# Optimization experiments

Measured on AMD Instinct MI355X. Metric: run time of the kernel, lower is better.

The kernel has to match this reference:

```python
import jax, jax.numpy as jnp
import numpy as np
import math

FREQS = jnp.array([1., 2., 4., 8., 7., 5.], dtype=jnp.float32)  # default frequencies


def setup_inputs() -> dict:
    key = jax.random.key(0)
    k1, k2, k3 = jax.random.split(key, 3)
    B, N, H, F = 8, 4096, 256, 6
    x = jax.random.normal(k1, (B, N, H), dtype=jnp.float32)
    t = jax.random.uniform(k2, (B, 1), dtype=jnp.float32) * (2.0 * math.pi)
    oscillators = jax.random.normal(k3, (F, H, H), dtype=jnp.float32) * 0.1
    # phase_shifts[i] = i / F * pi, broadcast over hidden dim (matches torch init)
    phase_shifts = jnp.broadcast_to(
        (jnp.arange(F, dtype=jnp.float32) / F * math.pi)[:, None], (F, H)
    ).copy()
    return {"x": x, "t": t, "oscillators": oscillators, "phase_shifts": phase_shifts}


def reference(x, t, oscillators, phase_shifts):
    # resonator[b, f, h] = sin(freq_f * t[b, 0] + phase[f, h])
    res = jnp.sin(FREQS[None, :, None] * t[:, :, None] + phase_shifts[None, :, :])  # [B, F, H]
    # result[b, n, k] = sum_f (x[b, n, :] @ W_f)[k] * res[b, f, k]
    return jnp.einsum('bnh,fhk,bfk->bnk', x, oscillators, res)
```

## Files before the change

kernel.cpp:

```cpp
#include <hip/hip_runtime.h>
#include <hip/hip_bf16.h>


#define B_  8
#define N_  4096
#define H_  256

typedef __attribute__((ext_vector_type(8))) short s8v;
typedef __attribute__((ext_vector_type(4))) float f4v;

__global__ __launch_bounds__(256) void build_w(
    const float* __restrict__ osc,
    const float* __restrict__ t,
    const float* __restrict__ phase,
    __hip_bfloat16* __restrict__ Wt)
{
    const float freqs[6] = {1.f, 2.f, 4.f, 8.f, 7.f, 5.f};
    __shared__ float tr[16 * 68];

    const int b  = blockIdx.z;
    const int n0 = blockIdx.y * 64;
    const int h0 = blockIdx.x * 128;
    const int tid = threadIdx.x;

    const float tb = t[b];
    const int nr = (tid & 15) * 4;
    const int hr = tid >> 4;
    float s[6][4];
#pragma unroll
    for (int f = 0; f < 6; ++f)
#pragma unroll
        for (int j = 0; j < 4; ++j)
            s[f][j] = __sinf(freqs[f] * tb + phase[f * 256 + n0 + nr + j]);

    const int nw = tid >> 2;
    const int hw = (tid & 3) * 4;
    __hip_bfloat16* wout = Wt + (size_t)b * 65536 + (size_t)(n0 + nw) * 256 + h0;

    for (int hp = 0; hp < 8; ++hp) {
        const int h = h0 + hp * 16 + hr;
        float4 acc = make_float4(0.f, 0.f, 0.f, 0.f);
#pragma unroll
        for (int f = 0; f < 6; ++f) {
            float4 o = *(const float4*)&osc[f * 65536 + h * 256 + n0 + nr];
            acc.x += o.x * s[f][0];
            acc.y += o.y * s[f][1];
            acc.z += o.z * s[f][2];
            acc.w += o.w * s[f][3];
        }
        __syncthreads();
        *(float4*)&tr[hr * 68 + nr] = acc;
        __syncthreads();
        float v0 = tr[(hw + 0) * 68 + nw];
        float v1 = tr[(hw + 1) * 68 + nw];
        float v2 = tr[(hw + 2) * 68 + nw];
        float v3 = tr[(hw + 3) * 68 + nw];
        union { __hip_bfloat162 h2[2]; unsigned long long q; } cv;
        cv.h2[0] = __float22bfloat162_rn(make_float2(v0, v1));
        cv.h2[1] = __float22bfloat162_rn(make_float2(v2, v3));
        *(unsigned long long*)(wout + hp * 16 + hw) = cv.q;
    }
}

#define LDST 40

__global__ __launch_bounds__(512, 4) void gemm(
    const float* __restrict__ X,
    const __hip_bfloat16* __restrict__ Wt,
    float* __restrict__ out)
{
    __shared__ short As[64 * LDST];
    __shared__ short Bs[256 * LDST];

    const int b     = blockIdx.y;
    const int mTile = blockIdx.x;

    const int tid    = threadIdx.x;
    const int lane   = tid & 63;
    const int wave   = tid >> 6;
    const int lane15 = lane & 15;
    const int quad   = lane >> 4;
    const int wm     = wave >> 2;
    const int wn     = wave & 3;

    const float* Xb          = X   + (size_t)b * N_ * H_ + (size_t)mTile * 64 * H_;
    const __hip_bfloat16* Wb = Wt  + (size_t)b * H_ * H_;
    float* Ob                = out + (size_t)b * N_ * H_ + (size_t)mTile * 64 * H_;

    const int arow = tid >> 3;
    const int aseg = tid & 7;
    const float* pa = Xb + (size_t)arow * H_ + aseg * 4;

    const int brow = tid >> 1;
    const int bh   = tid & 1;
    const __hip_bfloat16* pb = Wb + (size_t)brow * H_ + bh * 16;

    f4v acc[2][4] = {};

    float4 av = *(const float4*)pa;
    uint4  bv0 = *(const uint4*)(pb);
    uint4  bv1 = *(const uint4*)(pb + 8);

    for (int it = 0; it < 8; ++it) {
        union { __hip_bfloat162 h2[2]; unsigned long long q; } cv;
        cv.h2[0] = __float22bfloat162_rn(make_float2(av.x, av.y));
        cv.h2[1] = __float22bfloat162_rn(make_float2(av.z, av.w));
        *(unsigned long long*)(&As[arow * LDST + aseg * 4]) = cv.q;
        *(uint4*)(&Bs[brow * LDST + bh * 16 + 0]) = bv0;
        *(uint4*)(&Bs[brow * LDST + bh * 16 + 8]) = bv1;
        __syncthreads();

        if (it < 7) {
            av  = *(const float4*)(pa + (it + 1) * 32);
            bv0 = *(const uint4*)(pb + (it + 1) * 32);
            bv1 = *(const uint4*)(pb + (it + 1) * 32 + 8);
        }

        s8v af[2], bf[4];
#pragma unroll
        for (int mt = 0; mt < 2; ++mt)
            af[mt] = *(const s8v*)(&As[(wm * 32 + mt * 16 + lane15) * LDST + quad * 8]);
#pragma unroll
        for (int nt = 0; nt < 4; ++nt)
            bf[nt] = *(const s8v*)(&Bs[(wn * 64 + nt * 16 + lane15) * LDST + quad * 8]);

#pragma unroll
        for (int mt = 0; mt < 2; ++mt)
#pragma unroll
            for (int nt = 0; nt < 4; ++nt)
                acc[mt][nt] = __builtin_amdgcn_mfma_f32_16x16x32_bf16(
                    af[mt], bf[nt], acc[mt][nt], 0, 0, 0);
        __syncthreads();
    }

#pragma unroll
    for (int mt = 0; mt < 2; ++mt) {
#pragma unroll
        for (int r = 0; r < 4; ++r) {
            int row = wm * 32 + mt * 16 + quad * 4 + r;
            float* po = Ob + (size_t)row * H_ + wn * 64 + lane15;
#pragma unroll
            for (int nt = 0; nt < 4; ++nt)
                po[nt * 16] = acc[mt][nt][r];
        }
    }
}

extern "C" void kernel_launch(void* const* d_in, const int* in_sizes, int n_in,
                              void* d_out, int out_size, void* d_ws, size_t ws_size,
                              hipStream_t stream) {
    const float* x     = (const float*)d_in[0];
    const float* t     = (const float*)d_in[1];
    const float* osc   = (const float*)d_in[2];
    const float* phase = (const float*)d_in[3];
    __hip_bfloat16* Wt = (__hip_bfloat16*)d_ws;
    float* out = (float*)d_out;

    dim3 gw(2, 4, 8);
    build_w<<<gw, 256, 0, stream>>>(osc, t, phase, Wt);

    dim3 gg(64, 8);
    gemm<<<gg, 512, 0, stream>>>(x, Wt, out);
}
```

Before: 101.3 us.

## Load MFMA fragments directly from global memory, bypassing LDS staging

The GEMM now has each lane load its A and B MFMA fragments straight from global memory into registers and convert A to bf16 in place. This removes the shared-memory tiles and both __syncthreads per K step. The cost is redundant global loads: each X row is read by all 4 wn waves and each W row by both wm waves, which relies on L1/L2 to absorb the duplication. Global access patterns also become 32-byte segments spread across rows, and register use grows from holding next-iteration prefetches.

```diff
diff --git a/kernel.cpp b/kernel.cpp
--- a/kernel.cpp
+++ b/kernel.cpp
@@ -62,16 +62,20 @@
     }
 }
 
-#define LDST 40
+__device__ __forceinline__ s8v cvt_frag(float4 lo, float4 hi) {
+    union { __hip_bfloat162 h2[4]; s8v v; } cv;
+    cv.h2[0] = __float22bfloat162_rn(make_float2(lo.x, lo.y));
+    cv.h2[1] = __float22bfloat162_rn(make_float2(lo.z, lo.w));
+    cv.h2[2] = __float22bfloat162_rn(make_float2(hi.x, hi.y));
+    cv.h2[3] = __float22bfloat162_rn(make_float2(hi.z, hi.w));
+    return cv.v;
+}
 
 __global__ __launch_bounds__(512, 4) void gemm(
     const float* __restrict__ X,
     const __hip_bfloat16* __restrict__ Wt,
     float* __restrict__ out)
 {
-    __shared__ short As[64 * LDST];
-    __shared__ short Bs[256 * LDST];
-
     const int b     = blockIdx.y;
     const int mTile = blockIdx.x;
 
@@ -83,54 +87,59 @@
     const int wm     = wave >> 2;
     const int wn     = wave & 3;
 
-    const float* Xb          = X   + (size_t)b * N_ * H_ + (size_t)mTile * 64 * H_;
-    const __hip_bfloat16* Wb = Wt  + (size_t)b * H_ * H_;
-    float* Ob                = out + (size_t)b * N_ * H_ + (size_t)mTile * 64 * H_;
-
-    const int arow = tid >> 3;
-    const int aseg = tid & 7;
-    const float* pa = Xb + (size_t)arow * H_ + aseg * 4;
-
-    const int brow = tid >> 1;
-    const int bh   = tid & 1;
-    const __hip_bfloat16* pb = Wb + (size_t)brow * H_ + bh * 16;
+    const float* pa = X + (size_t)b * N_ * H_
+                        + (size_t)(mTile * 64 + wm * 32 + lane15) * H_ + quad * 8;
+    const __hip_bfloat16* pb = Wt + (size_t)b * H_ * H_
+                        + (size_t)(wn * 64 + lane15) * H_ + quad * 8;
+    float* Ob = out + (size_t)b * N_ * H_ + (size_t)(mTile * 64) * H_;
 
     f4v acc[2][4] = {};
 
-    float4 av = *(const float4*)pa;
-    uint4  bv0 = *(const uint4*)(pb);
-    uint4  bv1 = *(const uint4*)(pb + 8);
+    float4 aLo[2], aHi[2];
+    uint4  bc[4];
+
+#pragma unroll
+    for (int mt = 0; mt < 2; ++mt) {
+        aLo[mt] = *(const float4*)(pa + mt * 16 * H_);
+        aHi[mt] = *(const float4*)(pa + mt * 16 * H_ + 4);
+    }
+#pragma unroll
+    for (int nt = 0; nt < 4; ++nt)
+        bc[nt] = *(const uint4*)(pb + nt * 16 * H_);
 
     for (int it = 0; it < 8; ++it) {
-        union { __hip_bfloat162 h2[2]; unsigned long long q; } cv;
-        cv.h2[0] = __float22bfloat162_rn(make_float2(av.x, av.y));
-        cv.h2[1] = __float22bfloat162_rn(make_float2(av.z, av.w));
-        *(unsigned long long*)(&As[arow * LDST + aseg * 4]) = cv.q;
-        *(uint4*)(&Bs[brow * LDST + bh * 16 + 0]) = bv0;
-        *(uint4*)(&Bs[brow * LDST + bh * 16 + 8]) = bv1;
-        __syncthreads();
-
+        float4 nLo[2], nHi[2];
+        uint4  nB[4];
         if (it < 7) {
-            av  = *(const float4*)(pa + (it + 1) * 32);
-            bv0 = *(const uint4*)(pb + (it + 1) * 32);
-            bv1 = *(const uint4*)(pb + (it + 1) * 32 + 8);
+            const int k = (it + 1) * 32;
+#pragma unroll
+            for (int mt = 0; mt < 2; ++mt) {
+                nLo[mt] = *(const float4*)(pa + mt * 16 * H_ + k);
+                nHi[mt] = *(const float4*)(pa + mt * 16 * H_ + k + 4);
+            }
+#pragma unroll
+            for (int nt = 0; nt < 4; ++nt)
+                nB[nt] = *(const uint4*)(pb + nt * 16 * H_ + k);
         }
 
-        s8v af[2], bf[4];
+        s8v af[2];
 #pragma unroll
         for (int mt = 0; mt < 2; ++mt)
-            af[mt] = *(const s8v*)(&As[(wm * 32 + mt * 16 + lane15) * LDST + quad * 8]);
-#pragma unroll
-        for (int nt = 0; nt < 4; ++nt)
-            bf[nt] = *(const s8v*)(&Bs[(wn * 64 + nt * 16 + lane15) * LDST + quad * 8]);
+            af[mt] = cvt_frag(aLo[mt], aHi[mt]);
 
 #pragma unroll
         for (int mt = 0; mt < 2; ++mt)
 #pragma unroll
             for (int nt = 0; nt < 4; ++nt)
                 acc[mt][nt] = __builtin_amdgcn_mfma_f32_16x16x32_bf16(
-                    af[mt], bf[nt], acc[mt][nt], 0, 0, 0);
-        __syncthreads();
+                    af[mt], *(const s8v*)&bc[nt], acc[mt][nt], 0, 0, 0);
+
+        if (it < 7) {
+#pragma unroll
+            for (int mt = 0; mt < 2; ++mt) { aLo[mt] = nLo[mt]; aHi[mt] = nHi[mt]; }
+#pragma unroll
+            for (int nt = 0; nt < 4; ++nt) bc[nt] = nB[nt];
+        }
     }
 
 #pragma unroll
```

Measured after the change: 115.0 us. +13.5%, slower.
